# Optimization experiments

Measured on AMD Instinct MI355X. Metric: run time of the kernel, lower is better.

Reference implementation:

```python
import jax, jax.numpy as jnp
import numpy as np

B, T, D, DH, DFF = 4, 2048, 1024, 1024, 4096


def setup_inputs() -> dict:
    key = jax.random.key(0)
    ks = jax.random.split(key, 8)
    s = 0.02
    return {
        "x": jax.random.normal(ks[0], (B, T, D), jnp.float32),
        "ln1_g": jnp.ones((D,), jnp.float32),
        "ln1_b": jnp.zeros((D,), jnp.float32),
        "W_q": jax.random.normal(ks[1], (D, DH), jnp.float32) * s,
        "b_q": jnp.zeros((DH,), jnp.float32),
        "W_k": jax.random.normal(ks[2], (D, DH), jnp.float32) * s,
        "b_k": jnp.zeros((DH,), jnp.float32),
        "W_v": jax.random.normal(ks[3], (D, DH), jnp.float32) * s,
        "b_v": jnp.zeros((DH,), jnp.float32),
        "ln2_g": jnp.ones((D,), jnp.float32),
        "ln2_b": jnp.zeros((D,), jnp.float32),
        "W_in": jax.random.normal(ks[4], (D, DFF), jnp.float32) * s,
        "b_in": jnp.zeros((DFF,), jnp.float32),
        "W_out": jax.random.normal(ks[5], (DFF, D), jnp.float32) * s,
        "b_out": jnp.zeros((D,), jnp.float32),
    }


def _layernorm(x, g, b, eps=1e-5):
    mu = jnp.mean(x, axis=-1, keepdims=True)
    var = jnp.var(x, axis=-1, keepdims=True)
    return (x - mu) * jax.lax.rsqrt(var + eps) * g + b


def reference(x, ln1_g, ln1_b, W_q, b_q, W_k, b_k, W_v, b_v,
              ln2_g, ln2_b, W_in, b_in, W_out, b_out):
    # --- attention branch (pre-LN) ---
    h = _layernorm(x, ln1_g, ln1_b)                      # [B,T,D]
    Q = h @ W_q + b_q                                    # [B,T,DH]
    K = h @ W_k + b_k
    V = h @ W_v + b_v
    scale = 1.0 / jnp.sqrt(jnp.asarray(K.shape[-1], h.dtype))
    att = jnp.einsum("btd,bsd->bts", Q, K) * scale       # [B,T,T]
    # NOTE: source calls att.masked_fill(...) without assignment -> mask
    # is discarded; faithfully no causal mask applied here.
    att = jax.nn.softmax(att, axis=-1)
    attn_out = jnp.einsum("bts,bsd->btd", att, V)        # [B,T,DH]
    x = x + attn_out
    # --- MLP branch (pre-LN) ---
    h2 = _layernorm(x, ln2_g, ln2_b)
    ff = jax.nn.gelu(h2 @ W_in + b_in, approximate=False)
    x = x + (ff @ W_out + b_out)
    return x
```

## Files before the change

kernel.cpp:

```cpp
#include <hip/hip_runtime.h>
#include <hip/hip_bf16.h>

#define B_    4
#define T_    2048
#define D_    1024
#define DH_   1024
#define DFF_  4096
#define MTOT  (B_ * T_)

using f32x4  = __attribute__((ext_vector_type(4))) float;
using bf16x8 = __attribute__((ext_vector_type(8))) short;

__device__ __forceinline__ unsigned short f2bf(float f) {
    unsigned u = __builtin_bit_cast(unsigned, f);
    u += 0x7fffu + ((u >> 16) & 1u);
    return (unsigned short)(u >> 16);
}
__device__ __forceinline__ float bf2f(unsigned short h) {
    unsigned u = ((unsigned)h) << 16;
    return __builtin_bit_cast(float, u);
}

__device__ __forceinline__ void gload16(const short* g, short* l) {
    __builtin_amdgcn_global_load_lds(
        (const __attribute__((address_space(1))) unsigned int*)g,
        (__attribute__((address_space(3))) unsigned int*)l, 16, 0, 0);
}

__global__ __launch_bounds__(256) void transp_f32_bf16(
    const float* __restrict__ src, short* __restrict__ dst, int K, int N) {
    __shared__ float tile[32][33];
    int tk = blockIdx.y * 32, tn = blockIdx.x * 32;
    int tx = threadIdx.x & 31, ty = threadIdx.x >> 5;
#pragma unroll
    for (int i = 0; i < 4; i++) {
        int r = ty + i * 8;
        tile[r][tx] = src[(size_t)(tk + r) * N + tn + tx];
    }
    __syncthreads();
#pragma unroll
    for (int i = 0; i < 4; i++) {
        int r = ty + i * 8;
        dst[(size_t)(tn + r) * K + tk + tx] = f2bf(tile[tx][r]);
    }
}

__global__ void copyv(const float* __restrict__ s, float* __restrict__ d, int n) {
    int i = blockIdx.x * blockDim.x + threadIdx.x;
    if (i < n) d[i] = s[i];
}

__global__ __launch_bounds__(256) void ln_rows(
    const float* __restrict__ x, const float* __restrict__ g,
    const float* __restrict__ bta, short* __restrict__ out) {
    int row = blockIdx.x;
    const float* xr = x + (size_t)row * D_;
    int t = threadIdx.x;
    float4 v = *(const float4*)(xr + t * 4);
    float s  = v.x + v.y + v.z + v.w;
    float s2 = v.x * v.x + v.y * v.y + v.z * v.z + v.w * v.w;
#pragma unroll
    for (int off = 1; off < 64; off <<= 1) {
        s  += __shfl_xor(s, off);
        s2 += __shfl_xor(s2, off);
    }
    __shared__ float as_[4], as2_[4];
    int wave = t >> 6, lane = t & 63;
    if (lane == 0) { as_[wave] = s; as2_[wave] = s2; }
    __syncthreads();
    s  = as_[0] + as_[1] + as_[2] + as_[3];
    s2 = as2_[0] + as2_[1] + as2_[2] + as2_[3];
    float mean = s * (1.0f / D_);
    float var  = s2 * (1.0f / D_) - mean * mean;
    float rstd = rsqrtf(var + 1e-5f);
    float4 gv = *(const float4*)(g + t * 4);
    float4 bv = *(const float4*)(bta + t * 4);
    short4 o;
    o.x = f2bf((v.x - mean) * rstd * gv.x + bv.x);
    o.y = f2bf((v.y - mean) * rstd * gv.y + bv.y);
    o.z = f2bf((v.z - mean) * rstd * gv.z + bv.z);
    o.w = f2bf((v.w - mean) * rstd * gv.w + bv.w);
    *(short4*)(out + (size_t)row * D_ + t * 4) = o;
}

template<int BIAS_MODE, int ACT, int RES, int OUT_BF16>
__global__ __launch_bounds__(256, 2) void gemmT(
    const short* __restrict__ A, int lda, long long sA,
    const short* __restrict__ Bt, int ldb, long long sB,
    void* __restrict__ C, int ldc, long long sC,
    const float* __restrict__ bias,
    const float* __restrict__ res, int ldr, long long sR,
    int K) {
    extern __shared__ short smem_[];
    short* shA = smem_;
    short* shB = smem_ + 24576;

    int gx = gridDim.x, gy = gridDim.y;
    int n2d = gx * gy;
    int nwg = n2d * gridDim.z;
    int lid = blockIdx.x + gx * (blockIdx.y + gy * blockIdx.z);
    int q = nwg >> 3, rq = nwg & 7, xcd = lid & 7, i_ = lid >> 3;
    int nid = (xcd < rq ? xcd * (q + 1) : rq * (q + 1) + (xcd - rq) * q) + i_;
    int z = nid / n2d, r2d = nid % n2d;
    int sw = gy << 2;
    int strip = r2d / sw, rr = r2d % sw;
    int by = rr >> 2, bx = (strip << 2) + (rr & 3);

    int bm = by * 256, bn = bx * 128;
    const short* gA = A  + (size_t)z * sA + (size_t)bm * lda;
    const short* gB = Bt + (size_t)z * sB + (size_t)bn * ldb;
    int tid = threadIdx.x, lane = tid & 63, w = tid >> 6;
    int wr = w >> 1, wc = w & 1;

    int rbase = tid >> 2;
    int gcol  = ((((tid & 3) << 4) ^ (((rbase >> 1) & 3) << 4)) >> 1);
    const short* pA[4]; const short* pB[2];
#pragma unroll
    for (int c = 0; c < 4; c++)
        pA[c] = gA + (size_t)(c * 64 + rbase) * lda + gcol;
#pragma unroll
    for (int c = 0; c < 2; c++)
        pB[c] = gB + (size_t)(c * 64 + rbase) * ldb + gcol;

    int aoff[8], boff[4];
#pragma unroll
    for (int f = 0; f < 8; f++) {
        int row = wr * 128 + f * 16 + (lane & 15);
        aoff[f] = row * 64 + (((lane >> 4) * 16) ^ (((row >> 1) & 3) << 4));
    }
#pragma unroll
    for (int f = 0; f < 4; f++) {
        int row = wc * 64 + f * 16 + (lane & 15);
        boff[f] = row * 64 + (((lane >> 4) * 16) ^ (((row >> 1) & 3) << 4));
    }

    int nk = K >> 5;
    f32x4 acc[8][4] = {};

#pragma unroll
    for (int s = 0; s < 2; s++) {
#pragma unroll
        for (int c = 0; c < 4; c++)
            gload16(pA[c] + s * 32, shA + s * 8192 + c * 2048 + tid * 8);
#pragma unroll
        for (int c = 0; c < 2; c++)
            gload16(pB[c] + s * 32, shB + s * 4096 + c * 2048 + tid * 8);
    }
    asm volatile("s_waitcnt vmcnt(6)" ::: "memory");
    __builtin_amdgcn_s_barrier();

    bf16x8 aA[4], aB[4], b0[4], b1[4];
    {
        const char* s0A = (const char*)shA;
        const char* s0B = (const char*)shB;
#pragma unroll
        for (int f = 0; f < 4; f++) aA[f] = *(const bf16x8*)(s0A + aoff[f]);
#pragma unroll
        for (int f = 0; f < 4; f++) b0[f] = *(const bf16x8*)(s0B + boff[f]);
        asm volatile("s_waitcnt lgkmcnt(0)" ::: "memory");
    }

#define MF(r_, av, bv) \
    acc[r_][0] = __builtin_amdgcn_mfma_f32_16x16x32_bf16(av, bv[0], acc[r_][0], 0, 0, 0); \
    acc[r_][1] = __builtin_amdgcn_mfma_f32_16x16x32_bf16(av, bv[1], acc[r_][1], 0, 0, 0); \
    acc[r_][2] = __builtin_amdgcn_mfma_f32_16x16x32_bf16(av, bv[2], acc[r_][2], 0, 0, 0); \
    acc[r_][3] = __builtin_amdgcn_mfma_f32_16x16x32_bf16(av, bv[3], acc[r_][3], 0, 0, 0);

#define TILE(T, BUSE, BREAD) { \
    int t = (T); \
    const char* sA_  = (const char*)(shA + (t % 3) * 8192); \
    const char* sA1_ = (const char*)(shA + ((t + 1) % 3) * 8192); \
    const char* sB1_ = (const char*)(shB + ((t + 1) % 3) * 4096); \
    short* wA2 = shA + ((t + 2) % 3) * 8192; \
    short* wB2 = shB + ((t + 2) % 3) * 4096; \
    int ks = (t + 2 < nk ? t + 2 : nk - 1) << 5; \
     \
    aB[0] = *(const bf16x8*)(sA_ + aoff[4]); \
    aB[1] = *(const bf16x8*)(sA_ + aoff[5]); \
    aB[2] = *(const bf16x8*)(sA_ + aoff[6]); \
    aB[3] = *(const bf16x8*)(sA_ + aoff[7]); \
    gload16(pA[0] + ks, wA2 + 0 * 2048 + tid * 8); \
    gload16(pA[1] + ks, wA2 + 1 * 2048 + tid * 8); \
    asm volatile("s_waitcnt lgkmcnt(4)" ::: "memory"); \
    __builtin_amdgcn_sched_barrier(0); \
    __builtin_amdgcn_s_setprio(1); \
    MF(0, aA[0], BUSE) MF(1, aA[1], BUSE) MF(2, aA[2], BUSE) MF(3, aA[3], BUSE) \
    __builtin_amdgcn_s_setprio(0); \
    asm volatile("s_waitcnt vmcnt(2)" ::: "memory"); \
    __builtin_amdgcn_s_barrier(); \
     \
    aA[0] = *(const bf16x8*)(sA1_ + aoff[0]); \
    aA[1] = *(const bf16x8*)(sA1_ + aoff[1]); \
    aA[2] = *(const bf16x8*)(sA1_ + aoff[2]); \
    aA[3] = *(const bf16x8*)(sA1_ + aoff[3]); \
    BREAD[0] = *(const bf16x8*)(sB1_ + boff[0]); \
    BREAD[1] = *(const bf16x8*)(sB1_ + boff[1]); \
    BREAD[2] = *(const bf16x8*)(sB1_ + boff[2]); \
    BREAD[3] = *(const bf16x8*)(sB1_ + boff[3]); \
    gload16(pA[2] + ks, wA2 + 2 * 2048 + tid * 8); \
    gload16(pA[3] + ks, wA2 + 3 * 2048 + tid * 8); \
    gload16(pB[0] + ks, wB2 + 0 * 2048 + tid * 8); \
    gload16(pB[1] + ks, wB2 + 1 * 2048 + tid * 8); \
    asm volatile("s_waitcnt lgkmcnt(8)" ::: "memory"); \
    __builtin_amdgcn_sched_barrier(0); \
    __builtin_amdgcn_s_setprio(1); \
    MF(4, aB[0], BUSE) MF(5, aB[1], BUSE) MF(6, aB[2], BUSE) MF(7, aB[3], BUSE) \
    __builtin_amdgcn_s_setprio(0); \
    __builtin_amdgcn_s_barrier(); }

    for (int tp = 0; tp < nk; tp += 2) {
        TILE(tp,     b0, b1)
        TILE(tp + 1, b1, b0)
    }
#undef TILE
#undef MF
    asm volatile("s_waitcnt vmcnt(0)" ::: "memory");
    __syncthreads();

    size_t zc = (size_t)z * (size_t)sC;
    float* lpart = (float*)smem_;
#pragma unroll
    for (int fr = 0; fr < 8; fr++) {
        float pr[4] = {0.f, 0.f, 0.f, 0.f};
        float s8[4];
        if (RES == 2) {
#pragma unroll
            for (int r_ = 0; r_ < 4; r_++) {
                int row = bm + wr * 128 + fr * 16 + (lane >> 4) * 4 + r_;
                float s = 0.f;
#pragma unroll
                for (int i = 0; i < 16; i++) s += bias[((size_t)z * 16 + i) * 2048 + row];
                s8[r_] = 1.0f / s;
            }
        }
#pragma unroll
        for (int fn = 0; fn < 4; fn++) {
            int colc = bn + wc * 64 + fn * 16 + (lane & 15);
#pragma unroll
            for (int r_ = 0; r_ < 4; r_++) {
                int row = bm + wr * 128 + fr * 16 + (lane >> 4) * 4 + r_;
                float v = acc[fr][fn][r_];
                if (BIAS_MODE == 1) v += bias[colc];
                else if (BIAS_MODE == 2) v += bias[row];
                if (ACT == 1) v = 0.5f * v * (1.0f + erff(v * 0.70710678118654752f));
                if (ACT == 2) {
                    v = expf(v * 0.03125f);
                    unsigned short us = f2bf(v);
                    ((short*)C)[zc + (size_t)row * ldc + colc] = (short)us;
                    pr[r_] += bf2f(us);
                    continue;
                }
                if (RES == 1) v += res[(size_t)z * sR + (size_t)row * ldr + colc];
                if (RES == 2) v = v * s8[r_] + res[(size_t)z * sR + (size_t)row * ldr + colc];
                if (OUT_BF16) ((short*)C)[zc + (size_t)row * ldc + colc] = f2bf(v);
                else          ((float*)C)[zc + (size_t)row * ldc + colc] = v;
            }
        }
        if (ACT == 2) {
#pragma unroll
            for (int m_ = 1; m_ < 16; m_ <<= 1) {
#pragma unroll
                for (int r_ = 0; r_ < 4; r_++) pr[r_] += __shfl_xor(pr[r_], m_);
            }
            if ((lane & 15) == 0) {
#pragma unroll
                for (int r_ = 0; r_ < 4; r_++)
                    lpart[wc * 256 + wr * 128 + fr * 16 + (lane >> 4) * 4 + r_] = pr[r_];
            }
        }
    }
    if (ACT == 2) {
        __syncthreads();
        if (tid < 256) {
            float s = lpart[tid] + lpart[256 + tid];
            ((float*)res)[((size_t)z * 16 + bx) * 2048 + bm + tid] = s;
        }
    }
}

#define SHB 73728

extern "C" void kernel_launch(void* const* d_in, const int* in_sizes, int n_in,
                              void* d_out, int out_size, void* d_ws, size_t ws_size,
                              hipStream_t stream) {
    const float* x    = (const float*)d_in[0];
    const float* ln1g = (const float*)d_in[1];
    const float* ln1b = (const float*)d_in[2];
    const float* Wq   = (const float*)d_in[3];
    const float* bq   = (const float*)d_in[4];
    const float* Wk   = (const float*)d_in[5];
    const float* bk   = (const float*)d_in[6];
    const float* Wv   = (const float*)d_in[7];
    const float* bv   = (const float*)d_in[8];
    const float* ln2g = (const float*)d_in[9];
    const float* ln2b = (const float*)d_in[10];
    const float* Win  = (const float*)d_in[11];
    const float* bin  = (const float*)d_in[12];
    const float* Wout = (const float*)d_in[13];
    const float* bout = (const float*)d_in[14];

    char* ws = (char*)d_ws;
    size_t off = 0;
    auto alloc = [&](size_t bytes) {
        void* p = ws + off;
        off += (bytes + 255) & ~(size_t)255;
        return p;
    };
    short* WqkT  = (short*)alloc((size_t)2048 * 1024 * 2);
    short* WvT   = (short*)alloc((size_t)1024 * 1024 * 2);
    short* WinT  = (short*)alloc((size_t)4096 * 1024 * 2);
    short* WoutT = (short*)alloc((size_t)1024 * 4096 * 2);
    float* bqk   = (float*)alloc((size_t)2048 * 4);
    short* h     = (short*)alloc((size_t)MTOT * 1024 * 2);
    short* QK    = (short*)alloc((size_t)MTOT * 2048 * 2);
    short* VT    = (short*)alloc((size_t)1024 * 8192 * 2);
    float* S     = (float*)alloc((size_t)4 * 2048 * 2048 * 4);
    float* x1    = (float*)alloc((size_t)MTOT * 1024 * 4);
    float* rowsums = (float*)alloc((size_t)4 * 16 * 2048 * 4);
    (void)ws_size; (void)in_sizes; (void)n_in; (void)out_size;

    hipFuncSetAttribute((const void*)gemmT<1,0,0,1>, hipFuncAttributeMaxDynamicSharedMemorySize, SHB);
    hipFuncSetAttribute((const void*)gemmT<2,0,0,1>, hipFuncAttributeMaxDynamicSharedMemorySize, SHB);
    hipFuncSetAttribute((const void*)gemmT<0,2,0,1>, hipFuncAttributeMaxDynamicSharedMemorySize, SHB);
    hipFuncSetAttribute((const void*)gemmT<0,0,2,0>, hipFuncAttributeMaxDynamicSharedMemorySize, SHB);
    hipFuncSetAttribute((const void*)gemmT<1,1,0,1>, hipFuncAttributeMaxDynamicSharedMemorySize, SHB);
    hipFuncSetAttribute((const void*)gemmT<1,0,1,0>, hipFuncAttributeMaxDynamicSharedMemorySize, SHB);

    transp_f32_bf16<<<dim3(32, 32), 256, 0, stream>>>(Wq, WqkT, 1024, 1024);
    transp_f32_bf16<<<dim3(32, 32), 256, 0, stream>>>(Wk, WqkT + (size_t)1024 * 1024, 1024, 1024);
    transp_f32_bf16<<<dim3(32, 32), 256, 0, stream>>>(Wv, WvT, 1024, 1024);
    transp_f32_bf16<<<dim3(128, 32), 256, 0, stream>>>(Win, WinT, 1024, 4096);
    transp_f32_bf16<<<dim3(32, 128), 256, 0, stream>>>(Wout, WoutT, 4096, 1024);
    copyv<<<4, 256, 0, stream>>>(bq, bqk, 1024);
    copyv<<<4, 256, 0, stream>>>(bk, bqk + 1024, 1024);

    ln_rows<<<MTOT, 256, 0, stream>>>(x, ln1g, ln1b, h);

    gemmT<1, 0, 0, 1><<<dim3(16, 32, 1), 256, SHB, stream>>>(
        h, 1024, 0, WqkT, 1024, 0, QK, 2048, 0, bqk, nullptr, 0, 0, 1024);

    gemmT<2, 0, 0, 1><<<dim3(64, 4, 1), 256, SHB, stream>>>(
        WvT, 1024, 0, h, 1024, 0, VT, 8192, 0, bv, nullptr, 0, 0, 1024);

    gemmT<0, 2, 0, 1><<<dim3(16, 8, 4), 256, SHB, stream>>>(
        QK, 2048, 4194304LL, QK + 1024, 2048, 4194304LL,
        (short*)S, 4096, 8388608LL, nullptr, (const float*)rowsums, 0, 0, 1024);

    gemmT<0, 0, 2, 0><<<dim3(8, 8, 4), 256, SHB, stream>>>(
        (short*)S, 4096, 8388608LL, VT, 8192, 2048LL,
        x1, 1024, 2097152LL, rowsums, x, 1024, 2097152LL, 2048);

    ln_rows<<<MTOT, 256, 0, stream>>>(x1, ln2g, ln2b, h);

    short* ff = (short*)S;
    gemmT<1, 1, 0, 1><<<dim3(32, 32, 1), 256, SHB, stream>>>(
        h, 1024, 0, WinT, 1024, 0, ff, 4096, 0, bin, nullptr, 0, 0, 1024);

    gemmT<1, 0, 1, 0><<<dim3(8, 32, 1), 256, SHB, stream>>>(
        ff, 4096, 0, WoutT, 4096, 0, (float*)d_out, 1024, 0, bout,
        x1, 1024, 0, 4096);
}
```

Baseline: 413.7 us.

## Switch GEMM to 512-thread blocks with 256-wide tiles and 4-stage LDS pipeline

The GEMM kernel becomes templated on N fragments per wave (NB). It moves to 512 threads (8 waves, 2x4) and uses 256x256 tiles for the wide GEMMs, keeping 256x128 for the others. The LDS ring buffer grows from 3 to 4 stages with 3 tiles prefetched, and the split A/B fragment loads are replaced by a full register double buffer of all A and B fragments. The aim is more reuse per loaded byte and deeper latency hiding. In exchange it uses much more LDS (128KB), which may limit occupancy to one block per CU despite launch_bounds(512,2), and the softmax rowsum partials now come from 8 column tiles instead of 16.

New measurement: 388.5 us. -6.1%, faster.

```diff
diff --git a/kernel.cpp b/kernel.cpp
--- a/kernel.cpp
+++ b/kernel.cpp
@@ -83,17 +83,18 @@
     *(short4*)(out + (size_t)row * D_ + t * 4) = o;
 }
 
-template<int BIAS_MODE, int ACT, int RES, int OUT_BF16>
-__global__ __launch_bounds__(256, 2) void gemmT(
+template<int NB, int BIAS_MODE, int ACT, int RES, int OUT_BF16>
+__global__ __launch_bounds__(512, 2) void gemmT(
     const short* __restrict__ A, int lda, long long sA,
     const short* __restrict__ Bt, int ldb, long long sB,
     void* __restrict__ C, int ldc, long long sC,
     const float* __restrict__ bias,
     const float* __restrict__ res, int ldr, long long sR,
     int K) {
+    constexpr int BSLOT = (NB == 4 ? 8192 : 4096);
     extern __shared__ short smem_[];
     short* shA = smem_;
-    short* shB = smem_ + 24576;
+    short* shB = smem_ + 32768;
 
     int gx = gridDim.x, gy = gridDim.y;
     int n2d = gx * gy;
@@ -106,114 +107,87 @@
     int strip = r2d / sw, rr = r2d % sw;
     int by = rr >> 2, bx = (strip << 2) + (rr & 3);
 
-    int bm = by * 256, bn = bx * 128;
+    int bm = by * 256, bn = bx * (64 * NB);
     const short* gA = A  + (size_t)z * sA + (size_t)bm * lda;
     const short* gB = Bt + (size_t)z * sB + (size_t)bn * ldb;
     int tid = threadIdx.x, lane = tid & 63, w = tid >> 6;
-    int wr = w >> 1, wc = w & 1;
+    int wr = w >> 2, wc = w & 3;
 
     int rbase = tid >> 2;
-    int gcol  = ((((tid & 3) << 4) ^ (((rbase >> 1) & 3) << 4)) >> 1);
-    const short* pA[4]; const short* pB[2];
-#pragma unroll
-    for (int c = 0; c < 4; c++)
-        pA[c] = gA + (size_t)(c * 64 + rbase) * lda + gcol;
+    int gcol  = ((((tid & 3) << 4) ^ ((rbase & 6) << 3)) >> 1);
+    const short* pA[2]; const short* pB[2];
 #pragma unroll
     for (int c = 0; c < 2; c++)
-        pB[c] = gB + (size_t)(c * 64 + rbase) * ldb + gcol;
+        pA[c] = gA + (size_t)(c * 128 + rbase) * lda + gcol;
+    pB[0] = gB + (size_t)rbase * ldb + gcol;
+    if constexpr (NB == 4) pB[1] = gB + (size_t)(128 + rbase) * ldb + gcol;
 
     int aoff[8], boff[4];
 #pragma unroll
     for (int f = 0; f < 8; f++) {
         int row = wr * 128 + f * 16 + (lane & 15);
-        aoff[f] = row * 64 + (((lane >> 4) * 16) ^ (((row >> 1) & 3) << 4));
-    }
-#pragma unroll
-    for (int f = 0; f < 4; f++) {
-        int row = wc * 64 + f * 16 + (lane & 15);
-        boff[f] = row * 64 + (((lane >> 4) * 16) ^ (((row >> 1) & 3) << 4));
+        aoff[f] = row * 64 + (((lane >> 4) * 16) ^ ((row & 6) << 3));
+    }
+#pragma unroll
+    for (int f = 0; f < NB; f++) {
+        int row = wc * (16 * NB) + f * 16 + (lane & 15);
+        boff[f] = row * 64 + (((lane >> 4) * 16) ^ ((row & 6) << 3));
     }
 
     int nk = K >> 5;
-    f32x4 acc[8][4] = {};
-
-#pragma unroll
-    for (int s = 0; s < 2; s++) {
-#pragma unroll
-        for (int c = 0; c < 4; c++)
-            gload16(pA[c] + s * 32, shA + s * 8192 + c * 2048 + tid * 8);
-#pragma unroll
-        for (int c = 0; c < 2; c++)
-            gload16(pB[c] + s * 32, shB + s * 4096 + c * 2048 + tid * 8);
-    }
-    asm volatile("s_waitcnt vmcnt(6)" ::: "memory");
+    f32x4 acc[8][NB] = {};
+
+#pragma unroll
+    for (int s = 0; s < 3; s++) {
+        short* dA = shA + s * 8192;
+        short* dB = shB + s * BSLOT;
+        gload16(pA[0] + s * 32, dA + tid * 8);
+        gload16(pA[1] + s * 32, dA + 4096 + tid * 8);
+        gload16(pB[0] + s * 32, dB + tid * 8);
+        if constexpr (NB == 4) gload16(pB[1] + s * 32, dB + 4096 + tid * 8);
+    }
+    if constexpr (NB == 4) asm volatile("s_waitcnt vmcnt(4)" ::: "memory");
+    else                   asm volatile("s_waitcnt vmcnt(3)" ::: "memory");
     __builtin_amdgcn_s_barrier();
 
-    bf16x8 aA[4], aB[4], b0[4], b1[4];
-    {
-        const char* s0A = (const char*)shA;
-        const char* s0B = (const char*)shB;
-#pragma unroll
-        for (int f = 0; f < 4; f++) aA[f] = *(const bf16x8*)(s0A + aoff[f]);
-#pragma unroll
-        for (int f = 0; f < 4; f++) b0[f] = *(const bf16x8*)(s0B + boff[f]);
-        asm volatile("s_waitcnt lgkmcnt(0)" ::: "memory");
-    }
-
-#define MF(r_, av, bv) \
-    acc[r_][0] = __builtin_amdgcn_mfma_f32_16x16x32_bf16(av, bv[0], acc[r_][0], 0, 0, 0); \
-    acc[r_][1] = __builtin_amdgcn_mfma_f32_16x16x32_bf16(av, bv[1], acc[r_][1], 0, 0, 0); \
-    acc[r_][2] = __builtin_amdgcn_mfma_f32_16x16x32_bf16(av, bv[2], acc[r_][2], 0, 0, 0); \
-    acc[r_][3] = __builtin_amdgcn_mfma_f32_16x16x32_bf16(av, bv[3], acc[r_][3], 0, 0, 0);
-
-#define TILE(T, BUSE, BREAD) { \
+    bf16x8 cA[8], cB[4], nA[8], nB[4];
+#pragma unroll
+    for (int f = 0; f < 8; f++) cA[f] = *(const bf16x8*)((const char*)shA + aoff[f]);
+#pragma unroll
+    for (int f = 0; f < NB; f++) cB[f] = *(const bf16x8*)((const char*)shB + boff[f]);
+
+#define MFROW(r_, av, bv) \
+    _Pragma("unroll") \
+    for (int n_ = 0; n_ < NB; n_++) \
+        acc[r_][n_] = __builtin_amdgcn_mfma_f32_16x16x32_bf16(av, bv[n_], acc[r_][n_], 0, 0, 0);
+
+#define TILE(T, uA, uB, vA, vB) { \
     int t = (T); \
-    const char* sA_  = (const char*)(shA + (t % 3) * 8192); \
-    const char* sA1_ = (const char*)(shA + ((t + 1) % 3) * 8192); \
-    const char* sB1_ = (const char*)(shB + ((t + 1) % 3) * 4096); \
-    short* wA2 = shA + ((t + 2) % 3) * 8192; \
-    short* wB2 = shB + ((t + 2) % 3) * 4096; \
-    int ks = (t + 2 < nk ? t + 2 : nk - 1) << 5; \
-     \
-    aB[0] = *(const bf16x8*)(sA_ + aoff[4]); \
-    aB[1] = *(const bf16x8*)(sA_ + aoff[5]); \
-    aB[2] = *(const bf16x8*)(sA_ + aoff[6]); \
-    aB[3] = *(const bf16x8*)(sA_ + aoff[7]); \
-    gload16(pA[0] + ks, wA2 + 0 * 2048 + tid * 8); \
-    gload16(pA[1] + ks, wA2 + 1 * 2048 + tid * 8); \
-    asm volatile("s_waitcnt lgkmcnt(4)" ::: "memory"); \
-    __builtin_amdgcn_sched_barrier(0); \
-    __builtin_amdgcn_s_setprio(1); \
-    MF(0, aA[0], BUSE) MF(1, aA[1], BUSE) MF(2, aA[2], BUSE) MF(3, aA[3], BUSE) \
-    __builtin_amdgcn_s_setprio(0); \
-    asm volatile("s_waitcnt vmcnt(2)" ::: "memory"); \
-    __builtin_amdgcn_s_barrier(); \
-     \
-    aA[0] = *(const bf16x8*)(sA1_ + aoff[0]); \
-    aA[1] = *(const bf16x8*)(sA1_ + aoff[1]); \
-    aA[2] = *(const bf16x8*)(sA1_ + aoff[2]); \
-    aA[3] = *(const bf16x8*)(sA1_ + aoff[3]); \
-    BREAD[0] = *(const bf16x8*)(sB1_ + boff[0]); \
-    BREAD[1] = *(const bf16x8*)(sB1_ + boff[1]); \
-    BREAD[2] = *(const bf16x8*)(sB1_ + boff[2]); \
-    BREAD[3] = *(const bf16x8*)(sB1_ + boff[3]); \
-    gload16(pA[2] + ks, wA2 + 2 * 2048 + tid * 8); \
-    gload16(pA[3] + ks, wA2 + 3 * 2048 + tid * 8); \
-    gload16(pB[0] + ks, wB2 + 0 * 2048 + tid * 8); \
-    gload16(pB[1] + ks, wB2 + 1 * 2048 + tid * 8); \
-    asm volatile("s_waitcnt lgkmcnt(8)" ::: "memory"); \
-    __builtin_amdgcn_sched_barrier(0); \
-    __builtin_amdgcn_s_setprio(1); \
-    MF(4, aB[0], BUSE) MF(5, aB[1], BUSE) MF(6, aB[2], BUSE) MF(7, aB[3], BUSE) \
-    __builtin_amdgcn_s_setprio(0); \
+    const char* sA1 = (const char*)(shA + ((t + 1) & 3) * 8192); \
+    const char* sB1 = (const char*)(shB + ((t + 1) & 3) * BSLOT); \
+    short* wA = shA + ((t + 3) & 3) * 8192; \
+    short* wB = shB + ((t + 3) & 3) * BSLOT; \
+    int kk = (t + 3 < nk ? t + 3 : nk - 1) << 5; \
+    _Pragma("unroll") \
+    for (int f = 0; f < 8; f++) vA[f] = *(const bf16x8*)(sA1 + aoff[f]); \
+    _Pragma("unroll") \
+    for (int f = 0; f < NB; f++) vB[f] = *(const bf16x8*)(sB1 + boff[f]); \
+    gload16(pA[0] + kk, wA + tid * 8); \
+    gload16(pA[1] + kk, wA + 4096 + tid * 8); \
+    gload16(pB[0] + kk, wB + tid * 8); \
+    if constexpr (NB == 4) gload16(pB[1] + kk, wB + 4096 + tid * 8); \
+    MFROW(0, uA[0], uB) MFROW(1, uA[1], uB) MFROW(2, uA[2], uB) MFROW(3, uA[3], uB) \
+    MFROW(4, uA[4], uB) MFROW(5, uA[5], uB) MFROW(6, uA[6], uB) MFROW(7, uA[7], uB) \
+    if constexpr (NB == 4) asm volatile("s_waitcnt vmcnt(4)" ::: "memory"); \
+    else                   asm volatile("s_waitcnt vmcnt(3)" ::: "memory"); \
     __builtin_amdgcn_s_barrier(); }
 
     for (int tp = 0; tp < nk; tp += 2) {
-        TILE(tp,     b0, b1)
-        TILE(tp + 1, b1, b0)
+        TILE(tp,     cA, cB, nA, nB)
+        TILE(tp + 1, nA, nB, cA, cB)
     }
 #undef TILE
-#undef MF
+#undef MFROW
     asm volatile("s_waitcnt vmcnt(0)" ::: "memory");
     __syncthreads();
 
@@ -229,13 +203,13 @@
                 int row = bm + wr * 128 + fr * 16 + (lane >> 4) * 4 + r_;
                 float s = 0.f;
 #pragma unroll
-                for (int i = 0; i < 16; i++) s += bias[((size_t)z * 16 + i) * 2048 + row];
+                for (int i = 0; i < 8; i++) s += bias[((size_t)z * 8 + i) * 2048 + row];
                 s8[r_] = 1.0f / s;
             }
         }
 #pragma unroll
-        for (int fn = 0; fn < 4; fn++) {
-            int colc = bn + wc * 64 + fn * 16 + (lane & 15);
+        for (int fn = 0; fn < NB; fn++) {
+            int colc = bn + wc * (16 * NB) + fn * 16 + (lane & 15);
 #pragma unroll
             for (int r_ = 0; r_ < 4; r_++) {
                 int row = bm + wr * 128 + fr * 16 + (lane >> 4) * 4 + r_;
@@ -272,13 +246,14 @@
     if (ACT == 2) {
         __syncthreads();
         if (tid < 256) {
-            float s = lpart[tid] + lpart[256 + tid];
-            ((float*)res)[((size_t)z * 16 + bx) * 2048 + bm + tid] = s;
+            float s = lpart[tid] + lpart[256 + tid] + lpart[512 + tid] + lpart[768 + tid];
+            ((float*)res)[((size_t)z * 8 + bx) * 2048 + bm + tid] = s;
         }
     }
 }
 
-#define SHB 73728
+#define SHB4 131072
+#define SHB2 98304
 
 extern "C" void kernel_launch(void* const* d_in, const int* in_sizes, int n_in,
                               void* d_out, int out_size, void* d_ws, size_t ws_size,
@@ -316,15 +291,15 @@
     short* VT    = (short*)alloc((size_t)1024 * 8192 * 2);
     float* S     = (float*)alloc((size_t)4 * 2048 * 2048 * 4);
     float* x1    = (float*)alloc((size_t)MTOT * 1024 * 4);
-    float* rowsums = (float*)alloc((size_t)4 * 16 * 2048 * 4);
+    float* rowsums = (float*)alloc((size_t)4 * 8 * 2048 * 4);
     (void)ws_size; (void)in_sizes; (void)n_in; (void)out_size;
 
-    hipFuncSetAttribute((const void*)gemmT<1,0,0,1>, hipFuncAttributeMaxDynamicSharedMemorySize, SHB);
-    hipFuncSetAttribute((const void*)gemmT<2,0,0,1>, hipFuncAttributeMaxDynamicSharedMemorySize, SHB);
-    hipFuncSetAttribute((const void*)gemmT<0,2,0,1>, hipFuncAttributeMaxDynamicSharedMemorySize, SHB);
-    hipFuncSetAttribute((const void*)gemmT<0,0,2,0>, hipFuncAttributeMaxDynamicSharedMemorySize, SHB);
-    hipFuncSetAttribute((const void*)gemmT<1,1,0,1>, hipFuncAttributeMaxDynamicSharedMemorySize, SHB);
-    hipFuncSetAttribute((const void*)gemmT<1,0,1,0>, hipFuncAttributeMaxDynamicSharedMemorySize, SHB);
+    hipFuncSetAttribute((const void*)gemmT<4,1,0,0,1>, hipFuncAttributeMaxDynamicSharedMemorySize, SHB4);
+    hipFuncSetAttribute((const void*)gemmT<4,0,2,0,1>, hipFuncAttributeMaxDynamicSharedMemorySize, SHB4);
+    hipFuncSetAttribute((const void*)gemmT<4,1,1,0,1>, hipFuncAttributeMaxDynamicSharedMemorySize, SHB4);
+    hipFuncSetAttribute((const void*)gemmT<2,2,0,0,1>, hipFuncAttributeMaxDynamicSharedMemorySize, SHB2);
+    hipFuncSetAttribute((const void*)gemmT<2,0,0,2,0>, hipFuncAttributeMaxDynamicSharedMemorySize, SHB2);
+    hipFuncSetAttribute((const void*)gemmT<2,1,0,1,0>, hipFuncAttributeMaxDynamicSharedMemorySize, SHB2);
 
     transp_f32_bf16<<<dim3(32, 32), 256, 0, stream>>>(Wq, WqkT, 1024, 1024);
     transp_f32_bf16<<<dim3(32, 32), 256, 0, stream>>>(Wk, WqkT + (size_t)1024 * 1024, 1024, 1024);
@@ -336,27 +311,27 @@
 
     ln_rows<<<MTOT, 256, 0, stream>>>(x, ln1g, ln1b, h);
 
-    gemmT<1, 0, 0, 1><<<dim3(16, 32, 1), 256, SHB, stream>>>(
+    gemmT<4, 1, 0, 0, 1><<<dim3(8, 32, 1), 512, SHB4, stream>>>(
         h, 1024, 0, WqkT, 1024, 0, QK, 2048, 0, bqk, nullptr, 0, 0, 1024);
 
-    gemmT<2, 0, 0, 1><<<dim3(64, 4, 1), 256, SHB, stream>>>(
+    gemmT<2, 2, 0, 0, 1><<<dim3(64, 4, 1), 512, SHB2, stream>>>(
         WvT, 1024, 0, h, 1024, 0, VT, 8192, 0, bv, nullptr, 0, 0, 1024);
 
-    gemmT<0, 2, 0, 1><<<dim3(16, 8, 4), 256, SHB, stream>>>(
+    gemmT<4, 0, 2, 0, 1><<<dim3(8, 8, 4), 512, SHB4, stream>>>(
         QK, 2048, 4194304LL, QK + 1024, 2048, 4194304LL,
         (short*)S, 4096, 8388608LL, nullptr, (const float*)rowsums, 0, 0, 1024);
 
-    gemmT<0, 0, 2, 0><<<dim3(8, 8, 4), 256, SHB, stream>>>(
+    gemmT<2, 0, 0, 2, 0><<<dim3(8, 8, 4), 512, SHB2, stream>>>(
         (short*)S, 4096, 8388608LL, VT, 8192, 2048LL,
         x1, 1024, 2097152LL, rowsums, x, 1024, 2097152LL, 2048);
 
     ln_rows<<<MTOT, 256, 0, stream>>>(x1, ln2g, ln2b, h);
 
     short* ff = (short*)S;
-    gemmT<1, 1, 0, 1><<<dim3(32, 32, 1), 256, SHB, stream>>>(
+    gemmT<4, 1, 1, 0, 1><<<dim3(16, 32, 1), 512, SHB4, stream>>>(
         h, 1024, 0, WinT, 1024, 0, ff, 4096, 0, bin, nullptr, 0, 0, 1024);
 
-    gemmT<1, 0, 1, 0><<<dim3(8, 32, 1), 256, SHB, stream>>>(
+    gemmT<2, 1, 0, 1, 0><<<dim3(8, 32, 1), 512, SHB2, stream>>>(
         ff, 4096, 0, WoutT, 4096, 0, (float*)d_out, 1024, 0, bout,
         x1, 1024, 0, 4096);
 }
```
